# Performance work log

Measured on AMD Instinct MI355X. Metric: run time of the kernel, lower is better.

## Reference

```python
import jax, jax.numpy as jnp
import numpy as np

HID = 128

def _lstm_layer(x, w_ih, w_hh, b_ih, b_hh):
    # x: [N, T, I]; PyTorch gate order: i, f, g, o
    n = x.shape[0]
    xg = jnp.einsum('nti,gi->ntg', x, w_ih) + b_ih + b_hh  # [N, T, 4H]
    xg = jnp.transpose(xg, (1, 0, 2))                       # [T, N, 4H]

    def step(carry, xg_t):
        h, c = carry
        g = xg_t + h @ w_hh.T                               # [N, 4H]
        i, f, gg, o = jnp.split(g, 4, axis=-1)
        i = jax.nn.sigmoid(i)
        f = jax.nn.sigmoid(f)
        gg = jnp.tanh(gg)
        o = jax.nn.sigmoid(o)
        c = f * c + i * gg
        h = o * jnp.tanh(c)
        return (h, c), h

    h0 = jnp.zeros((n, HID), dtype=x.dtype)
    c0 = jnp.zeros((n, HID), dtype=x.dtype)
    (hn, cn), hs = jax.lax.scan(step, (h0, c0), xg)
    return jnp.transpose(hs, (1, 0, 2))                     # [N, T, H]


def setup_inputs() -> dict:
    key = jax.random.key(0)
    ks = jax.random.split(key, 12)
    N = 8192
    s0 = 1.0 / np.sqrt(HID)
    u = lambda k, shape: jax.random.uniform(k, shape, jnp.float32, -s0, s0)
    return {
        'x': jax.random.normal(ks[0], (N, 1, 28, 28), jnp.float32),
        'w_ih0': u(ks[1], (4 * HID, 28)),
        'w_hh0': u(ks[2], (4 * HID, HID)),
        'b_ih0': u(ks[3], (4 * HID,)),
        'b_hh0': u(ks[4], (4 * HID,)),
        'w_ih1': u(ks[5], (4 * HID, HID)),
        'w_hh1': u(ks[6], (4 * HID, HID)),
        'b_ih1': u(ks[7], (4 * HID,)),
        'b_hh1': u(ks[8], (4 * HID,)),
        'w_out': u(ks[9], (10, HID)),
        'b_out': u(ks[10], (10,)),
    }


def reference(x, w_ih0, w_hh0, b_ih0, b_hh0, w_ih1, w_hh1, b_ih1, b_hh1, w_out, b_out):
    n, c, h, w = x.shape
    # permute(0,2,3,1).reshape(n, h, w*c) -> [N, 28, 28]
    seq = jnp.transpose(x, (0, 2, 3, 1)).reshape(n, h, w * c)
    hs1 = _lstm_layer(seq, w_ih0, w_hh0, b_ih0, b_hh0)
    hs2 = _lstm_layer(hs1, w_ih1, w_hh1, b_ih1, b_hh1)
    out = hs2[:, -1, :] @ w_out.T + b_out                   # [N, 10]
    return out
```

## Files before the change

kernel.cpp:

```cpp
#include <hip/hip_runtime.h>


typedef short  short8   __attribute__((ext_vector_type(8)));
typedef float  float4_t __attribute__((ext_vector_type(4)));

#define WIH1_OFF 0
#define H0_OFF   131072
#define H1_OFF   147456
#define SMEM_SZ  163840

#define WPACK_SHORTS 212992u
#define XPACK_SHORTS 7340032u

#define LOG2E  1.4426950408889634f
#define TLOG2E 2.8853900817779268f

__device__ __forceinline__ unsigned short bf16r(float v) {
  union { float f; unsigned u; } x; x.f = v;
  unsigned r = x.u + 0x7fffu + ((x.u >> 16) & 1u);
  return (unsigned short)(r >> 16);
}
__device__ __forceinline__ float bf2f(unsigned short b) {
  union { unsigned u; float f; } x; x.u = ((unsigned)b) << 16;
  return x.f;
}
__device__ __forceinline__ float sig2(float xs) {
  return __builtin_amdgcn_rcpf(1.0f + __builtin_amdgcn_exp2f(-xs));
}
__device__ __forceinline__ float tanh2(float xs) {
  return 1.0f - 2.0f * __builtin_amdgcn_rcpf(__builtin_amdgcn_exp2f(xs) + 1.0f);
}
__device__ __forceinline__ unsigned cvt_pk_bf16(float lo, float hi) {
  unsigned u;
  asm("v_cvt_pk_bf16_f32 %0, %1, %2" : "=v"(u) : "v"(lo), "v"(hi));
  return u;
}

__global__ void pack_weights(const float* __restrict__ wih0, const float* __restrict__ whh0,
                             const float* __restrict__ wih1, const float* __restrict__ whh1,
                             unsigned short* __restrict__ dst)
{
  int e = blockIdx.x * 256 + threadIdx.x;
  const float* src; int K; int i;
  if      (e < 16384)  { src = wih0; K = 28;  i = e;          }
  else if (e < 81920)  { src = whh0; K = 128; i = e - 16384;  }
  else if (e < 147456) { src = wih1; K = 128; i = e - 81920;  }
  else if (e < 212992) { src = whh1; K = 128; i = e - 147456; }
  else return;
  int j = i & 7, lane = (i >> 3) & 63, tile = (i >> 9) & 31, kc = i >> 14;
  int row = tile * 16 + (lane & 15);
  int k = kc * 32 + ((lane >> 4) << 3) + j;
  float v = (k < K) ? src[row * K + k] : 0.0f;
  float s = ((tile >> 3) == 2) ? TLOG2E : LOG2E;
  dst[e] = bf16r(v * s);
}

__global__ void pack_x(const float* __restrict__ xg, unsigned* __restrict__ dst)
{
  unsigned d = blockIdx.x * 256 + threadIdx.x;
  if (d >= XPACK_SHORTS / 2) return;
  unsigned base = d * 2;
  int j    = base & 7;
  int lane = (base >> 3) & 63;
  int mt   = (base >> 9) & 1;
  unsigned bt = base >> 10;
  int t    = bt % 28;
  int blk  = bt / 28;
  int s    = blk * 32 + mt * 16 + (lane & 15);
  int k    = ((lane >> 4) << 3) + j;
  float v0 = 0.f, v1 = 0.f;
  if (k < 28) {
    const float* xs = xg + (size_t)s * 784 + t * 28 + k;
    v0 = xs[0]; v1 = xs[1];
  }
  dst[d] = (unsigned)bf16r(v0) | ((unsigned)bf16r(v1) << 16);
}

__global__ __launch_bounds__(512, 2)
void lstm_fused(const float* __restrict__ xg,
                const unsigned short* __restrict__ wpack,
                const unsigned short* __restrict__ xpk,
                const float* __restrict__ bih0, const float* __restrict__ bhh0,
                const float* __restrict__ bih1, const float* __restrict__ bhh1,
                const float* __restrict__ wout, const float* __restrict__ bout,
                float* __restrict__ out)
{
  extern __shared__ __align__(16) char smem[];

  const int tid  = threadIdx.x;
  const int lane = tid & 63;
  const int wave = tid >> 6;
  const bool isL0 = (wave < 4);
  const int gw   = wave & 3;
  const int q    = lane >> 4;
  const int mcol = lane & 15;
  const int n0   = blockIdx.x * 32;

  const short8* wp = (const short8*)wpack;

  short8 W[2][4][4];
  short8 WX[2][4];
  if (isL0) {
#pragma unroll
    for (int dgi = 0; dgi < 2; ++dgi) {
      int dg = gw * 2 + dgi;
#pragma unroll
      for (int g = 0; g < 4; ++g)
        WX[dgi][g] = wp[(g * 8 + dg) * 64 + lane];
#pragma unroll
      for (int kc = 0; kc < 4; ++kc)
#pragma unroll
        for (int g = 0; g < 4; ++g)
          W[dgi][kc][g] = wp[ 2048 + (kc * 32 + g * 8 + dg) * 64 + lane];
    }
  } else {
#pragma unroll
    for (int dgi = 0; dgi < 2; ++dgi) {
      int dg = gw * 2 + dgi;
#pragma unroll
      for (int kc = 0; kc < 4; ++kc)
#pragma unroll
        for (int g = 0; g < 4; ++g)
          W[dgi][kc][g] = wp[18432 + (kc * 32 + g * 8 + dg) * 64 + lane];
    }
  }

  {
    short8* dstp = (short8*)smem;
#pragma unroll
    for (int rr = 0; rr < 16; ++rr)
      dstp[rr * 512 + tid] = wp[10240 + rr * 512 + tid];
  }

  float bias[2][4];
#pragma unroll
  for (int dgi = 0; dgi < 2; ++dgi) {
    const int d = (gw * 2 + dgi) * 16 + mcol;
#pragma unroll
    for (int g = 0; g < 4; ++g) {
      float b = isL0 ? (bih0[g * 128 + d] + bhh0[g * 128 + d])
                     : (bih1[g * 128 + d] + bhh1[g * 128 + d]);
      bias[dgi][g] = b * ((g == 2) ? TLOG2E : LOG2E);
    }
  }

  {
    int* z0 = (int*)(smem + H0_OFF + 8192);
    int* z1 = (int*)(smem + H1_OFF + 8192);
#pragma unroll
    for (int rr = 0; rr < 4; ++rr) { z0[rr * 512 + tid] = 0; z1[rr * 512 + tid] = 0; }
  }

  __syncthreads();

  const short8* W1f = (const short8*)(smem + WIH1_OFF);
  const short8* XP  = (const short8*)xpk;

  int hconst[2];
#pragma unroll
  for (int dgi = 0; dgi < 2; ++dgi)
    hconst[dgi] = gw * 1024 + (((dgi << 1) | (mcol >> 3)) * 256) + q * 64 + (mcol & 7) * 2;

  float cc[2][2][4] = {{{0.f,0.f,0.f,0.f},{0.f,0.f,0.f,0.f}},
                       {{0.f,0.f,0.f,0.f},{0.f,0.f,0.f,0.f}}};

#pragma unroll 1
  for (int I = 0; I < 29; ++I) {
    if (isL0) {
      if (I < 28) {
        const short8* H0R = (const short8*)(smem + H0_OFF + (((I + 1) & 1) << 13));
        char*         h0w = smem + H0_OFF + ((I & 1) << 13);

        short8 xf[2];
        if (xpk) {
#pragma unroll
          for (int mt = 0; mt < 2; ++mt)
            xf[mt] = XP[((blockIdx.x * 28 + I) * 2 + mt) * 64 + lane];
        } else {
#pragma unroll
          for (int mt = 0; mt < 2; ++mt) {
            const float* xsrc = xg + (size_t)(n0 + mt * 16 + mcol) * 784 + I * 28 + q * 8;
            float4_t xa = *(const float4_t*)xsrc;
            const float* x2 = xsrc + ((q == 3) ? 0 : 4);
            float4_t xb = *(const float4_t*)x2;
            if (q == 3) xb = (float4_t){0.f, 0.f, 0.f, 0.f};
            short8 f;
#pragma unroll
            for (int j = 0; j < 4; ++j) {
              f[j]     = (short)bf16r(xa[j]);
              f[j + 4] = (short)bf16r(xb[j]);
            }
            xf[mt] = f;
          }
        }

#pragma unroll
        for (int dgi = 0; dgi < 2; ++dgi)
#pragma unroll
          for (int mt = 0; mt < 2; ++mt) {
            float4_t acc[4];
#pragma unroll
            for (int g = 0; g < 4; ++g)
              acc[g] = (float4_t){bias[dgi][g], bias[dgi][g], bias[dgi][g], bias[dgi][g]};
            __builtin_amdgcn_s_setprio(1);
#pragma unroll
            for (int kc = 0; kc < 4; ++kc) {
              short8 hf = H0R[(mt * 4 + kc) * 64 + lane];
#pragma unroll
              for (int g = 0; g < 4; ++g)
                acc[g] = __builtin_amdgcn_mfma_f32_16x16x32_bf16(hf, W[dgi][kc][g], acc[g], 0, 0, 0);
            }
#pragma unroll
            for (int g = 0; g < 4; ++g)
              acc[g] = __builtin_amdgcn_mfma_f32_16x16x32_bf16(xf[mt], WX[dgi][g], acc[g], 0, 0, 0);
            __builtin_amdgcn_s_setprio(0);
            float hv[4];
#pragma unroll
            for (int r = 0; r < 4; ++r) {
              float c = sig2(acc[1][r]) * cc[dgi][mt][r] + sig2(acc[0][r]) * tanh2(acc[2][r]);
              cc[dgi][mt][r] = c;
              hv[r] = sig2(acc[3][r]) * tanh2(c * TLOG2E);
            }
            unsigned u01 = cvt_pk_bf16(hv[0], hv[1]);
            unsigned u23 = cvt_pk_bf16(hv[2], hv[3]);
            char* base = h0w + mt * 4096 + hconst[dgi];
            *(unsigned short*)(base +  0) = (unsigned short)u01;
            *(unsigned short*)(base + 16) = (unsigned short)(u01 >> 16);
            *(unsigned short*)(base + 32) = (unsigned short)u23;
            *(unsigned short*)(base + 48) = (unsigned short)(u23 >> 16);
          }
      }
    } else {
      if (I > 0) {
        const short8* H0S = (const short8*)(smem + H0_OFF + (((I - 1) & 1) << 13));
        const short8* H1R = (const short8*)(smem + H1_OFF + ((I & 1) << 13));
        char*         h1w = smem + H1_OFF + (((I - 1) & 1) << 13);
#pragma unroll
        for (int dgi = 0; dgi < 2; ++dgi) {
          int dg = gw * 2 + dgi;
          float4_t acc[2][4];
#pragma unroll
          for (int mt = 0; mt < 2; ++mt)
#pragma unroll
            for (int g = 0; g < 4; ++g)
              acc[mt][g] = (float4_t){bias[dgi][g], bias[dgi][g], bias[dgi][g], bias[dgi][g]};
          __builtin_amdgcn_s_setprio(1);
#pragma unroll
          for (int kc = 0; kc < 4; ++kc)
#pragma unroll
            for (int mt = 0; mt < 2; ++mt) {
              short8 hf = H1R[(mt * 4 + kc) * 64 + lane];
#pragma unroll
              for (int g = 0; g < 4; ++g)
                acc[mt][g] = __builtin_amdgcn_mfma_f32_16x16x32_bf16(hf, W[dgi][kc][g], acc[mt][g], 0, 0, 0);
            }
#pragma unroll
          for (int kc = 0; kc < 4; ++kc) {
            short8 wf[4];
#pragma unroll
            for (int g = 0; g < 4; ++g)
              wf[g] = W1f[(kc * 32 + g * 8 + dg) * 64 + lane];
#pragma unroll
            for (int mt = 0; mt < 2; ++mt) {
              short8 hf = H0S[(mt * 4 + kc) * 64 + lane];
#pragma unroll
              for (int g = 0; g < 4; ++g)
                acc[mt][g] = __builtin_amdgcn_mfma_f32_16x16x32_bf16(hf, wf[g], acc[mt][g], 0, 0, 0);
            }
          }
          __builtin_amdgcn_s_setprio(0);
#pragma unroll
          for (int mt = 0; mt < 2; ++mt) {
            float hv[4];
#pragma unroll
            for (int r = 0; r < 4; ++r) {
              float c = sig2(acc[mt][1][r]) * cc[dgi][mt][r] + sig2(acc[mt][0][r]) * tanh2(acc[mt][2][r]);
              cc[dgi][mt][r] = c;
              hv[r] = sig2(acc[mt][3][r]) * tanh2(c * TLOG2E);
            }
            unsigned u01 = cvt_pk_bf16(hv[0], hv[1]);
            unsigned u23 = cvt_pk_bf16(hv[2], hv[3]);
            char* base = h1w + mt * 4096 + hconst[dgi];
            *(unsigned short*)(base +  0) = (unsigned short)u01;
            *(unsigned short*)(base + 16) = (unsigned short)(u01 >> 16);
            *(unsigned short*)(base + 32) = (unsigned short)u23;
            *(unsigned short*)(base + 48) = (unsigned short)(u23 >> 16);
          }
        }
      }
    }
    __syncthreads();
  }

  if (tid < 320) {
    const short8* H1f = (const short8*)(smem + H1_OFF + 8192);
    int s = tid / 10, o = tid - (tid / 10) * 10;
    float sum = bout[o];
#pragma unroll
    for (int kc = 0; kc < 4; ++kc)
#pragma unroll
      for (int sb = 0; sb < 4; ++sb) {
        short8 hv = H1f[((s >> 4) * 4 + kc) * 64 + sb * 16 + (s & 15)];
        int dbase = kc * 32 + sb * 8;
        float4_t w0 = *(const float4_t*)(wout + o * 128 + dbase);
        float4_t w1 = *(const float4_t*)(wout + o * 128 + dbase + 4);
#pragma unroll
        for (int j = 0; j < 4; ++j) {
          sum += bf2f((unsigned short)hv[j])     * w0[j];
          sum += bf2f((unsigned short)hv[j + 4]) * w1[j];
        }
      }
    out[(size_t)(n0 + s) * 10 + o] = sum;
  }
}

extern "C" void kernel_launch(void* const* d_in, const int* in_sizes, int n_in,
                              void* d_out, int out_size, void* d_ws, size_t ws_size,
                              hipStream_t stream) {
  const float* x    = (const float*)d_in[0];
  const float* wih0 = (const float*)d_in[1];
  const float* whh0 = (const float*)d_in[2];
  const float* bih0 = (const float*)d_in[3];
  const float* bhh0 = (const float*)d_in[4];
  const float* wih1 = (const float*)d_in[5];
  const float* whh1 = (const float*)d_in[6];
  const float* bih1 = (const float*)d_in[7];
  const float* bhh1 = (const float*)d_in[8];
  const float* wout = (const float*)d_in[9];
  const float* bout = (const float*)d_in[10];

  unsigned short* wp = (unsigned short*)d_ws;
  const size_t need = (size_t)(WPACK_SHORTS + XPACK_SHORTS) * 2;

  pack_weights<<<832, 256, 0, stream>>>(wih0, whh0, wih1, whh1, wp);

  const unsigned short* xpk = nullptr;
  if (ws_size >= need) {
    unsigned short* xp = wp + WPACK_SHORTS;
    pack_x<<<(XPACK_SHORTS / 2 + 255) / 256, 256, 0, stream>>>(x, (unsigned*)xp);
    xpk = xp;
  }

  lstm_fused<<<256, 512, SMEM_SZ, stream>>>(x, wp, xpk, bih0, bhh0, bih1, bhh1,
                                            wout, bout, (float*)d_out);
}
```

Before: 207.0 us.

## Drop x pre-pack kernel, convert x inline, merge sigmoid-tanh reciprocals

Removes the separate pack_x pass that wrote a bf16 copy of the input to workspace. The fused kernel now loads x in fp32 and converts it in-register with packed bf16 conversion instructions. It also merges each sigmoid·tanh product into a single reciprocal, saving a reciprocal per gate pair. The aim is to cut a whole kernel launch and its extra memory pass, at the cost of strided fp32 global loads on the layer-0 critical path and a product form that could overflow when exp2 gets large.

Result: faster. 199.0 us (-3.8%).

```diff
diff --git a/kernel.cpp b/kernel.cpp
--- a/kernel.cpp
+++ b/kernel.cpp
@@ -9,9 +9,6 @@
 #define H1_OFF   147456
 #define SMEM_SZ  163840
 
-#define WPACK_SHORTS 212992u
-#define XPACK_SHORTS 7340032u
-
 #define LOG2E  1.4426950408889634f
 #define TLOG2E 2.8853900817779268f
 
@@ -27,8 +24,9 @@
 __device__ __forceinline__ float sig2(float xs) {
   return __builtin_amdgcn_rcpf(1.0f + __builtin_amdgcn_exp2f(-xs));
 }
-__device__ __forceinline__ float tanh2(float xs) {
-  return 1.0f - 2.0f * __builtin_amdgcn_rcpf(__builtin_amdgcn_exp2f(xs) + 1.0f);
+__device__ __forceinline__ float sig_tanh2(float as, float B) {
+  return (B - 1.0f) * __builtin_amdgcn_rcpf(
+      (1.0f + __builtin_amdgcn_exp2f(-as)) * (B + 1.0f));
 }
 __device__ __forceinline__ unsigned cvt_pk_bf16(float lo, float hi) {
   unsigned u;
@@ -55,31 +53,9 @@
   dst[e] = bf16r(v * s);
 }
 
-__global__ void pack_x(const float* __restrict__ xg, unsigned* __restrict__ dst)
-{
-  unsigned d = blockIdx.x * 256 + threadIdx.x;
-  if (d >= XPACK_SHORTS / 2) return;
-  unsigned base = d * 2;
-  int j    = base & 7;
-  int lane = (base >> 3) & 63;
-  int mt   = (base >> 9) & 1;
-  unsigned bt = base >> 10;
-  int t    = bt % 28;
-  int blk  = bt / 28;
-  int s    = blk * 32 + mt * 16 + (lane & 15);
-  int k    = ((lane >> 4) << 3) + j;
-  float v0 = 0.f, v1 = 0.f;
-  if (k < 28) {
-    const float* xs = xg + (size_t)s * 784 + t * 28 + k;
-    v0 = xs[0]; v1 = xs[1];
-  }
-  dst[d] = (unsigned)bf16r(v0) | ((unsigned)bf16r(v1) << 16);
-}
-
 __global__ __launch_bounds__(512, 2)
 void lstm_fused(const float* __restrict__ xg,
                 const unsigned short* __restrict__ wpack,
-                const unsigned short* __restrict__ xpk,
                 const float* __restrict__ bih0, const float* __restrict__ bhh0,
                 const float* __restrict__ bih1, const float* __restrict__ bhh1,
                 const float* __restrict__ wout, const float* __restrict__ bout,
@@ -154,7 +130,6 @@
   __syncthreads();
 
   const short8* W1f = (const short8*)(smem + WIH1_OFF);
-  const short8* XP  = (const short8*)xpk;
 
   int hconst[2];
 #pragma unroll
@@ -172,26 +147,19 @@
         char*         h0w = smem + H0_OFF + ((I & 1) << 13);
 
         short8 xf[2];
-        if (xpk) {
-#pragma unroll
-          for (int mt = 0; mt < 2; ++mt)
-            xf[mt] = XP[((blockIdx.x * 28 + I) * 2 + mt) * 64 + lane];
-        } else {
-#pragma unroll
-          for (int mt = 0; mt < 2; ++mt) {
-            const float* xsrc = xg + (size_t)(n0 + mt * 16 + mcol) * 784 + I * 28 + q * 8;
-            float4_t xa = *(const float4_t*)xsrc;
-            const float* x2 = xsrc + ((q == 3) ? 0 : 4);
-            float4_t xb = *(const float4_t*)x2;
-            if (q == 3) xb = (float4_t){0.f, 0.f, 0.f, 0.f};
-            short8 f;
-#pragma unroll
-            for (int j = 0; j < 4; ++j) {
-              f[j]     = (short)bf16r(xa[j]);
-              f[j + 4] = (short)bf16r(xb[j]);
-            }
-            xf[mt] = f;
-          }
+#pragma unroll
+        for (int mt = 0; mt < 2; ++mt) {
+          const float* xsrc = xg + (size_t)(n0 + mt * 16 + mcol) * 784 + I * 28 + q * 8;
+          float4_t xa = *(const float4_t*)xsrc;
+          const float* x2 = xsrc + ((q == 3) ? 0 : 4);
+          float4_t xb = *(const float4_t*)x2;
+          if (q == 3) xb = (float4_t){0.f, 0.f, 0.f, 0.f};
+          union { short8 s; unsigned u[4]; } U;
+          U.u[0] = cvt_pk_bf16(xa[0], xa[1]);
+          U.u[1] = cvt_pk_bf16(xa[2], xa[3]);
+          U.u[2] = cvt_pk_bf16(xb[0], xb[1]);
+          U.u[3] = cvt_pk_bf16(xb[2], xb[3]);
+          xf[mt] = U.s;
         }
 
 #pragma unroll
@@ -217,9 +185,11 @@
             float hv[4];
 #pragma unroll
             for (int r = 0; r < 4; ++r) {
-              float c = sig2(acc[1][r]) * cc[dgi][mt][r] + sig2(acc[0][r]) * tanh2(acc[2][r]);
+              float Bg = __builtin_amdgcn_exp2f(acc[2][r]);
+              float c  = sig2(acc[1][r]) * cc[dgi][mt][r] + sig_tanh2(acc[0][r], Bg);
               cc[dgi][mt][r] = c;
-              hv[r] = sig2(acc[3][r]) * tanh2(c * TLOG2E);
+              float Bc = __builtin_amdgcn_exp2f(c * TLOG2E);
+              hv[r] = sig_tanh2(acc[3][r], Bc);
             }
             unsigned u01 = cvt_pk_bf16(hv[0], hv[1]);
             unsigned u23 = cvt_pk_bf16(hv[2], hv[3]);
@@ -274,9 +244,11 @@
             float hv[4];
 #pragma unroll
             for (int r = 0; r < 4; ++r) {
-              float c = sig2(acc[mt][1][r]) * cc[dgi][mt][r] + sig2(acc[mt][0][r]) * tanh2(acc[mt][2][r]);
+              float Bg = __builtin_amdgcn_exp2f(acc[mt][2][r]);
+              float c  = sig2(acc[mt][1][r]) * cc[dgi][mt][r] + sig_tanh2(acc[mt][0][r], Bg);
               cc[dgi][mt][r] = c;
-              hv[r] = sig2(acc[mt][3][r]) * tanh2(c * TLOG2E);
+              float Bc = __builtin_amdgcn_exp2f(c * TLOG2E);
+              hv[r] = sig_tanh2(acc[mt][3][r], Bc);
             }
             unsigned u01 = cvt_pk_bf16(hv[0], hv[1]);
             unsigned u23 = cvt_pk_bf16(hv[2], hv[3]);
@@ -330,17 +302,8 @@
   const float* bout = (const float*)d_in[10];
 
   unsigned short* wp = (unsigned short*)d_ws;
-  const size_t need = (size_t)(WPACK_SHORTS + XPACK_SHORTS) * 2;
 
   pack_weights<<<832, 256, 0, stream>>>(wih0, whh0, wih1, whh1, wp);
-
-  const unsigned short* xpk = nullptr;
-  if (ws_size >= need) {
-    unsigned short* xp = wp + WPACK_SHORTS;
-    pack_x<<<(XPACK_SHORTS / 2 + 255) / 256, 256, 0, stream>>>(x, (unsigned*)xp);
-    xpk = xp;
-  }
-
-  lstm_fused<<<256, 512, SMEM_SZ, stream>>>(x, wp, xpk, bih0, bhh0, bih1, bhh1,
+  lstm_fused<<<256, 512, SMEM_SZ, stream>>>(x, wp, bih0, bhh0, bih1, bhh1,
                                             wout, bout, (float*)d_out);
 }
```
